# Performance work log

Hardware: AMD Instinct MI355X
Metric: run time of the kernel (lower is better)

Reference implementation:

```python
import jax, jax.numpy as jnp
import numpy as np

# Fingertip landmark indices (end_ldmrk = [12,24,36,48,57] in flat coords -> landmarks {4,8,12,16,19})
_END_LANDMARKS = {4, 8, 12, 16, 19}

def _build_pairs():
    pairs = []
    for j in range(20):  # index in range(0, 60, 3) -> landmark j = index//3
        start = j + 1 if j in _END_LANDMARKS else j + 2  # skip adjacent landmark unless fingertip
        for k in range(start, 21):  # x in range(start, 63, 3) -> landmark k = x//3
            pairs.append((j, k))
    return np.asarray(pairs, dtype=np.int32)  # [195, 2]

_PAIRS = _build_pairs()
_I = jnp.asarray(_PAIRS[:, 0])  # [195]
_J = jnp.asarray(_PAIRS[:, 1])  # [195]


def setup_inputs() -> dict:
    key = jax.random.key(0)
    B = 1_000_000
    return {"tensor": jax.random.normal(key, (B, 63), dtype=jnp.float32)}


def reference(tensor):
    # tensor: [B, 63] = 21 landmarks x (x, y, z); distances use only x, y.
    B = tensor.shape[0]
    xy = tensor.reshape(B, 21, 3)[..., :2]          # [B, 21, 2]
    d = xy[:, _I, :] - xy[:, _J, :]                 # [B, 195, 2] only needed pairs
    feats = jnp.sqrt(jnp.sum(d * d, axis=-1))       # [B, 195] 2D Euclidean distances
    return jnp.concatenate([tensor, feats], axis=-1)  # [B, 258]
```

## Files before the change

kernel.cpp:

```cpp
#include <hip/hip_runtime.h>
#include <math.h>

#define ROWS 16
#define NPAIRS 195
#define NTHREADS 256
#define ROW_OUT 258
#define NLM 21
#define TILE_F (ROWS * ROW_OUT)
#define IN_F (ROWS * 63)
#define GRID 1024

typedef float f32x4 __attribute__((ext_vector_type(4)));

#define LDS_BARRIER() asm volatile("s_waitcnt lgkmcnt(0)\n\ts_barrier" ::: "memory")

struct CodeTab { unsigned int c[NPAIRS]; };

constexpr CodeTab make_codes() {
    CodeTab t{};
    int n = 0;
    for (int a = 0; a < 20; ++a) {
        bool tip = (a == 4) || (a == 8) || (a == 12) || (a == 16) || (a == 19);
        int start = tip ? a + 1 : a + 2;
        for (int b = start; b < 21; ++b) {
            t.c[n] = (unsigned int)a | ((unsigned int)b << 16);
            ++n;
        }
    }
    return t;
}

__constant__ CodeTab CODES = make_codes();

__device__ __forceinline__ void scatter_tile(float* __restrict__ tile,
                                             float2* __restrict__ xy2,
                                             const float v[4], int r0, int col,
                                             int lm, int c3) {
#pragma unroll
    for (int e = 0; e < 4; ++e) {
        tile[(r0 + 4 * e) * ROW_OUT + col] = v[e];
    }
    if (c3 == 0) {
#pragma unroll
        for (int e = 0; e < 4; ++e) xy2[(r0 + 4 * e) * NLM + lm].x = v[e];
    } else if (c3 == 1) {
#pragma unroll
        for (int e = 0; e < 4; ++e) xy2[(r0 + 4 * e) * NLM + lm].y = v[e];
    }
}

__device__ __forceinline__ void compute_dists(float* __restrict__ tile,
                                              const float2* __restrict__ xy2,
                                              int t) {
    const int r = t >> 4;
    const int q = t & 15;
    const float2* __restrict__ xr = xy2 + r * NLM;
    float* __restrict__ drow = tile + r * ROW_OUT + 63;
#pragma unroll
    for (int k = 0; k < 13; ++k) {
        const int p = q + (k << 4);
        if (k < 12 || q < 3) {
            const unsigned int c = CODES.c[p];
            const float2 a = xr[c & 0xffu];
            const float2 b = xr[c >> 16];
            const float dx = a.x - b.x;
            const float dy = a.y - b.y;
            drow[p] = __builtin_amdgcn_sqrtf(dx * dx + dy * dy);
        }
    }
}

__global__ __launch_bounds__(NTHREADS)
void HandKineticLayer_18545668784560_kernel(const float* __restrict__ in,
                                            float* __restrict__ out,
                                            int B) {
    __shared__ __align__(16) float tile[2][TILE_F];
    __shared__ float2 xy2[2][ROWS * NLM];

    const int t = threadIdx.x;
    const int ntiles = B / ROWS;

    const int r0 = t / 63;
    const int col = t - r0 * 63;
    const int lm = col / 3;
    const int c3 = col - lm * 3;

    const int tile0 = blockIdx.x;
    if (tile0 < ntiles) {
        if (t < 252) {
            const float* __restrict__ ip = in + (size_t)tile0 * IN_F + t;
            float v[4];
#pragma unroll
            for (int e = 0; e < 4; ++e)
                v[e] = __builtin_nontemporal_load(ip + 252 * e);
            scatter_tile(tile[0], xy2[0], v, r0, col, lm, c3);
        }
        LDS_BARRIER();
    }

    int i = 0;
    for (int tl = tile0; tl < ntiles; tl += GRID, ++i) {
        const int cur = i & 1;
        const int nxt = tl + GRID;
        float vn[4] = {0.f, 0.f, 0.f, 0.f};
        const bool have_next = (nxt < ntiles) && (t < 252);
        if (have_next) {
            const float* __restrict__ ip = in + (size_t)nxt * IN_F + t;
#pragma unroll
            for (int e = 0; e < 4; ++e)
                vn[e] = __builtin_nontemporal_load(ip + 252 * e);
        }

        compute_dists(tile[cur], xy2[cur], t);
        LDS_BARRIER();

        {
            const f32x4* __restrict__ tl4 =
                reinterpret_cast<const f32x4*>(&tile[cur][0]);
            f32x4* __restrict__ o4 =
                reinterpret_cast<f32x4*>(out + (size_t)tl * TILE_F);
#pragma unroll
            for (int k = t; k < TILE_F / 4; k += NTHREADS) {
                __builtin_nontemporal_store(tl4[k], &o4[k]);
            }
        }

        if (have_next) {
            scatter_tile(tile[cur ^ 1], xy2[cur ^ 1], vn, r0, col, lm, c3);
        }
        LDS_BARRIER();
    }

    const int rem = B - ntiles * ROWS;
    if (rem > 0 && blockIdx.x == (unsigned)(ntiles % GRID)) {
        const int rowBase = ntiles * ROWS;
        const int nelem = rem * 63;
        for (int g = t; g < nelem; g += NTHREADS) {
            const float val = in[(size_t)rowBase * 63 + g];
            const int row = g / 63;
            const int cc = g - row * 63;
            tile[0][row * ROW_OUT + cc] = val;
            const int lmm = cc / 3;
            const int cc3 = cc - lmm * 3;
            if (cc3 == 0) xy2[0][row * NLM + lmm].x = val;
            else if (cc3 == 1) xy2[0][row * NLM + lmm].y = val;
        }
        __syncthreads();
        const int total = rem * NPAIRS;
        for (int idx = t; idx < total; idx += NTHREADS) {
            const int row = idx / NPAIRS;
            const int p = idx - row * NPAIRS;
            const unsigned int c = CODES.c[p];
            const float2 a = xy2[0][row * NLM + (int)(c & 0xffu)];
            const float2 b = xy2[0][row * NLM + (int)(c >> 16)];
            const float dx = a.x - b.x;
            const float dy = a.y - b.y;
            tile[0][row * ROW_OUT + 63 + p] = __builtin_amdgcn_sqrtf(dx * dx + dy * dy);
        }
        __syncthreads();
        const int nout = rem * ROW_OUT;
        for (int k = t; k < nout; k += NTHREADS) {
            out[(size_t)rowBase * ROW_OUT + k] = tile[0][k];
        }
    }
}

extern "C" void kernel_launch(void* const* d_in, const int* in_sizes, int n_in,
                              void* d_out, int out_size, void* d_ws, size_t ws_size,
                              hipStream_t stream) {
    const float* in = (const float*)d_in[0];
    float* out = (float*)d_out;
    const int B = in_sizes[0] / 63;
    hipLaunchKernelGGL(HandKineticLayer_18545668784560_kernel,
                       dim3(GRID), dim3(NTHREADS), 0, stream,
                       in, out, B);
}
```

Baseline: 272.6 us.

## Single-buffer LDS tile, double grid size, and raise occupancy bound

Drops the LDS double buffer so each block uses about half the shared memory, and adds an extra barrier between the output store and the scatter of the next tile. The grid is doubled to 2048 blocks and launch bounds ask for 8 blocks per CU, so more blocks can be resident and hide memory latency. The cost is one more block-wide barrier per tile and less overlap inside a block. The custom waitcnt+barrier asm is replaced by __syncthreads.

```diff
diff --git a/kernel.cpp b/kernel.cpp
--- a/kernel.cpp
+++ b/kernel.cpp
@@ -8,11 +8,9 @@
 #define NLM 21
 #define TILE_F (ROWS * ROW_OUT)
 #define IN_F (ROWS * 63)
-#define GRID 1024
+#define GRID 2048
 
 typedef float f32x4 __attribute__((ext_vector_type(4)));
-
-#define LDS_BARRIER() asm volatile("s_waitcnt lgkmcnt(0)\n\ts_barrier" ::: "memory")
 
 struct CodeTab { unsigned int c[NPAIRS]; };
 
@@ -70,12 +68,12 @@
     }
 }
 
-__global__ __launch_bounds__(NTHREADS)
+__global__ __launch_bounds__(NTHREADS, 8)
 void HandKineticLayer_18545668784560_kernel(const float* __restrict__ in,
                                             float* __restrict__ out,
                                             int B) {
-    __shared__ __align__(16) float tile[2][TILE_F];
-    __shared__ float2 xy2[2][ROWS * NLM];
+    __shared__ __align__(16) float tile[TILE_F];
+    __shared__ float2 xy2[ROWS * NLM];
 
     const int t = threadIdx.x;
     const int ntiles = B / ROWS;
@@ -93,14 +91,12 @@
 #pragma unroll
             for (int e = 0; e < 4; ++e)
                 v[e] = __builtin_nontemporal_load(ip + 252 * e);
-            scatter_tile(tile[0], xy2[0], v, r0, col, lm, c3);
+            scatter_tile(tile, xy2, v, r0, col, lm, c3);
         }
-        LDS_BARRIER();
+        __syncthreads();
     }
 
-    int i = 0;
-    for (int tl = tile0; tl < ntiles; tl += GRID, ++i) {
-        const int cur = i & 1;
+    for (int tl = tile0; tl < ntiles; tl += GRID) {
         const int nxt = tl + GRID;
         float vn[4] = {0.f, 0.f, 0.f, 0.f};
         const bool have_next = (nxt < ntiles) && (t < 252);
@@ -111,12 +107,12 @@
                 vn[e] = __builtin_nontemporal_load(ip + 252 * e);
         }
 
-        compute_dists(tile[cur], xy2[cur], t);
-        LDS_BARRIER();
+        compute_dists(tile, xy2, t);
+        __syncthreads();
 
         {
             const f32x4* __restrict__ tl4 =
-                reinterpret_cast<const f32x4*>(&tile[cur][0]);
+                reinterpret_cast<const f32x4*>(&tile[0]);
             f32x4* __restrict__ o4 =
                 reinterpret_cast<f32x4*>(out + (size_t)tl * TILE_F);
 #pragma unroll
@@ -124,11 +120,12 @@
                 __builtin_nontemporal_store(tl4[k], &o4[k]);
             }
         }
+        __syncthreads();
 
         if (have_next) {
-            scatter_tile(tile[cur ^ 1], xy2[cur ^ 1], vn, r0, col, lm, c3);
+            scatter_tile(tile, xy2, vn, r0, col, lm, c3);
         }
-        LDS_BARRIER();
+        __syncthreads();
     }
 
     const int rem = B - ntiles * ROWS;
@@ -139,11 +136,11 @@
             const float val = in[(size_t)rowBase * 63 + g];
             const int row = g / 63;
             const int cc = g - row * 63;
-            tile[0][row * ROW_OUT + cc] = val;
+            tile[row * ROW_OUT + cc] = val;
             const int lmm = cc / 3;
             const int cc3 = cc - lmm * 3;
-            if (cc3 == 0) xy2[0][row * NLM + lmm].x = val;
-            else if (cc3 == 1) xy2[0][row * NLM + lmm].y = val;
+            if (cc3 == 0) xy2[row * NLM + lmm].x = val;
+            else if (cc3 == 1) xy2[row * NLM + lmm].y = val;
         }
         __syncthreads();
         const int total = rem * NPAIRS;
@@ -151,16 +148,16 @@
             const int row = idx / NPAIRS;
             const int p = idx - row * NPAIRS;
             const unsigned int c = CODES.c[p];
-            const float2 a = xy2[0][row * NLM + (int)(c & 0xffu)];
-            const float2 b = xy2[0][row * NLM + (int)(c >> 16)];
+            const float2 a = xy2[row * NLM + (int)(c & 0xffu)];
+            const float2 b = xy2[row * NLM + (int)(c >> 16)];
             const float dx = a.x - b.x;
             const float dy = a.y - b.y;
-            tile[0][row * ROW_OUT + 63 + p] = __builtin_amdgcn_sqrtf(dx * dx + dy * dy);
+            tile[row * ROW_OUT + 63 + p] = __builtin_amdgcn_sqrtf(dx * dx + dy * dy);
         }
         __syncthreads();
         const int nout = rem * ROW_OUT;
         for (int k = t; k < nout; k += NTHREADS) {
-            out[(size_t)rowBase * ROW_OUT + k] = tile[0][k];
+            out[(size_t)rowBase * ROW_OUT + k] = tile[k];
         }
     }
 }
```

Result: faster. 256.9 us (-5.8%).
